# Performance work log

Measured on AMD Instinct MI355X. Metric: run time of the kernel, lower is better.

Reference implementation:

```python
import jax, jax.numpy as jnp
import numpy as np
import math

B, S, D_IN, D_OUT, H = 2, 2048, 1024, 1024, 16
HD = D_OUT // H


def setup_inputs() -> dict:
    key = jax.random.key(0)
    ks = jax.random.split(key, 6)
    scale = 0.02
    return {
        "x": jax.random.normal(ks[0], (B, S, D_IN), dtype=jnp.float32),
        "Wq": jax.random.normal(ks[1], (D_IN, D_OUT), dtype=jnp.float32) * scale,
        "Wk": jax.random.normal(ks[2], (D_IN, D_OUT), dtype=jnp.float32) * scale,
        "Wv": jax.random.normal(ks[3], (D_IN, D_OUT), dtype=jnp.float32) * scale,
        "Wo": jax.random.normal(ks[4], (D_OUT, D_OUT), dtype=jnp.float32) * scale,
        "bo": jax.random.normal(ks[5], (D_OUT,), dtype=jnp.float32) * scale,
    }


def reference(x, Wq, Wk, Wv, Wo, bo):
    b, n, _ = x.shape
    # project and split heads -> [b, h, n, hd]
    q = (x @ Wq).reshape(b, n, H, HD).transpose(0, 2, 1, 3)
    k = (x @ Wk).reshape(b, n, H, HD).transpose(0, 2, 1, 3)
    v = (x @ Wv).reshape(b, n, H, HD).transpose(0, 2, 1, 3)
    # materialized [b, h, n, n] scores with causal mask (as in original)
    scores = jnp.einsum('bhqd,bhkd->bhqk', q, k)
    causal = jnp.tril(jnp.ones((n, n), dtype=bool))  # True = keep
    scores = jnp.where(causal, scores, -jnp.inf)
    attn = jax.nn.softmax(scores / math.sqrt(HD), axis=-1)
    ctx = jnp.einsum('bhqk,bhkd->bhqd', attn, v)
    ctx = ctx.transpose(0, 2, 1, 3).reshape(b, n, D_OUT)
    return ctx @ Wo + bo
```

## Files before the change

kernel.cpp:

```cpp
#include <hip/hip_runtime.h>
#include <hip/hip_bf16.h>
#include <math.h>

typedef __bf16 v8bf __attribute__((ext_vector_type(8)));
typedef __bf16 v4bf __attribute__((ext_vector_type(4)));
typedef short  v4s  __attribute__((ext_vector_type(4)));
typedef float  v4f  __attribute__((ext_vector_type(4)));
typedef unsigned short u16;

static_assert(sizeof(v8bf) == 16, "v8bf must be 16B");

__device__ __forceinline__ u16 f2bf(float f) {
  __hip_bfloat16 h = __float2bfloat16(f);
  return *reinterpret_cast<u16*>(&h);
}
__device__ __forceinline__ v4f mfma16(v8bf a, v8bf b, v4f c) {
  return __builtin_amdgcn_mfma_f32_16x16x32_bf16(a, b, c, 0, 0, 0);
}
__device__ __forceinline__ v4f mfma16k16(v4bf a, v4bf b, v4f c) {
#if __has_builtin(__builtin_amdgcn_mfma_f32_16x16x16_bf16)
  return __builtin_amdgcn_mfma_f32_16x16x16_bf16(a, b, c, 0, 0, 0);
#else
  union { v4bf f; v4s s; } ua, ub;
  ua.f = a; ub.f = b;
  return __builtin_amdgcn_mfma_f32_16x16x16bf16_1k(ua.s, ub.s, c, 0, 0, 0);
#endif
}
__device__ __forceinline__ void async16(const u16* g, u16* l) {
  __builtin_amdgcn_global_load_lds(
      (__attribute__((address_space(1))) void*)(void*)g,
      (__attribute__((address_space(3))) void*)l, 16, 0, 0);
}

__global__ void prep(const float* __restrict__ x, const float* __restrict__ Wq,
                     const float* __restrict__ Wk, const float* __restrict__ Wv,
                     const float* __restrict__ Wo, u16* __restrict__ Wt,
                     u16* __restrict__ xb) {
  int tx = threadIdx.x, ty = threadIdx.y;
  if (blockIdx.z == 4) {
    int bid = blockIdx.y * 32 + blockIdx.x;
    int i = (bid * 1024 + ty * 32 + tx) * 4;
    float4 v = *(const float4*)(x + i);
    ushort4 o;
    o.x = f2bf(v.x); o.y = f2bf(v.y); o.z = f2bf(v.z); o.w = f2bf(v.w);
    *(ushort4*)(xb + i) = o;
    return;
  }
  __shared__ float tile[32][33];
  const float* src = (blockIdx.z == 0) ? Wq : (blockIdx.z == 1) ? Wk : (blockIdx.z == 2) ? Wv : Wo;
  int k0 = blockIdx.x * 32, n0 = blockIdx.y * 32;
  tile[ty][tx] = src[(size_t)(k0 + ty) * 1024 + n0 + tx];
  __syncthreads();
  Wt[(size_t)(blockIdx.z * 1024 + n0 + ty) * 1024 + k0 + tx] = f2bf(tile[tx][ty]);
}

__device__ __forceinline__ void gemm_core(const u16* __restrict__ A, const u16* __restrict__ Bt,
                                          u16* sA, u16* sB, v4f acc[4][4], int bm, int bn) {
  const int t = threadIdx.x;
  const int w = t >> 6, l = t & 63;
  const int quad = l >> 4, low = l & 15;
  const int wm = (w & 1) * 64, wn = (w >> 1) * 64;
  const int rowA = bm * 128 + w * 32 + (l >> 2);
  const int rowB = bn * 128 + w * 32 + (l >> 2);
  const int col8 = (l & 3) * 8;
  u16* la = sA + w * 1024;
  u16* lb = sB + w * 1024;

  for (int kb = 0; kb < 1024; kb += 32) {
    async16(A + (size_t)rowA * 1024 + kb + col8, la);
    async16(A + (size_t)(rowA + 16) * 1024 + kb + col8, la + 512);
    async16(Bt + (size_t)rowB * 1024 + kb + col8, lb);
    async16(Bt + (size_t)(rowB + 16) * 1024 + kb + col8, lb + 512);
    __syncthreads();
    v8bf af[4], bfr[4];
#pragma unroll
    for (int i = 0; i < 4; i++)
      af[i] = *(const v8bf*)(sA + (wm + i * 16 + low) * 32 + quad * 8);
#pragma unroll
    for (int j = 0; j < 4; j++)
      bfr[j] = *(const v8bf*)(sB + (wn + j * 16 + low) * 32 + quad * 8);
#pragma unroll
    for (int i = 0; i < 4; i++)
#pragma unroll
      for (int j = 0; j < 4; j++)
        acc[i][j] = mfma16(af[i], bfr[j], acc[i][j]);
    __syncthreads();
  }
}

__global__ __launch_bounds__(256) void gemm_qkv(const u16* __restrict__ xb,
                                                const u16* __restrict__ Wt,
                                                u16* __restrict__ Qb,
                                                u16* __restrict__ Kb,
                                                u16* __restrict__ Vt) {
  __shared__ __align__(16) u16 sA[128 * 32];
  __shared__ __align__(16) u16 sB[128 * 32];
  v4f acc[4][4] = {};
  const int bm = blockIdx.x, bn = blockIdx.y;
  gemm_core(xb, Wt, sA, sB, acc, bm, bn);
  const int t = threadIdx.x, w = t >> 6, l = t & 63, quad = l >> 4, low = l & 15;
  const int wm = (w & 1) * 64, wn = (w >> 1) * 64;
  const int zone = (bn * 128) >> 10;
  const float qsc = (zone == 0) ? 0.18033688011112042f : 1.0f;
#pragma unroll
  for (int i = 0; i < 4; i++) {
    int m0 = bm * 128 + wm + i * 16 + quad * 4;
#pragma unroll
    for (int j = 0; j < 4; j++) {
      int nn = (bn * 128 + wn + j * 16 + low) & 1023;
      if (zone == 0) {
#pragma unroll
        for (int r = 0; r < 4; r++)
          Qb[(size_t)(m0 + r) * 1024 + nn] = f2bf(acc[i][j][r] * qsc);
      } else if (zone == 1) {
#pragma unroll
        for (int r = 0; r < 4; r++)
          Kb[(size_t)(m0 + r) * 1024 + nn] = f2bf(acc[i][j][r]);
      } else {
        int bb = m0 >> 11, s = m0 & 2047;
#pragma unroll
        for (int r = 0; r < 4; r++)
          Vt[(size_t)(bb * 1024 + nn) * 2048 + s + r] = f2bf(acc[i][j][r]);
      }
    }
  }
}

__global__ __launch_bounds__(256) void gemm_out(const u16* __restrict__ ctx,
                                                const u16* __restrict__ Wt,
                                                const float* __restrict__ bo,
                                                float* __restrict__ out) {
  __shared__ __align__(16) u16 sA[128 * 32];
  __shared__ __align__(16) u16 sB[64 * 32];
  const u16* Bt = Wt + (size_t)3072 * 1024;
  v4f acc[4][2] = {};
  const int bm = blockIdx.x, bn = blockIdx.y;
  const int t = threadIdx.x, w = t >> 6, l = t & 63, quad = l >> 4, low = l & 15;
  const int wm = (w & 1) * 64, wn = (w >> 1) * 32;
  const int rowA = bm * 128 + w * 32 + (l >> 2);
  const int rowB = bn * 64 + w * 16 + (l >> 2);
  const int col8 = (l & 3) * 8;
  u16* la = sA + w * 1024;
  u16* lb = sB + w * 512;

  for (int kb = 0; kb < 1024; kb += 32) {
    async16(ctx + (size_t)rowA * 1024 + kb + col8, la);
    async16(ctx + (size_t)(rowA + 16) * 1024 + kb + col8, la + 512);
    async16(Bt + (size_t)rowB * 1024 + kb + col8, lb);
    __syncthreads();
    v8bf af[4], bfr[2];
#pragma unroll
    for (int i = 0; i < 4; i++)
      af[i] = *(const v8bf*)(sA + (wm + i * 16 + low) * 32 + quad * 8);
#pragma unroll
    for (int j = 0; j < 2; j++)
      bfr[j] = *(const v8bf*)(sB + (wn + j * 16 + low) * 32 + quad * 8);
#pragma unroll
    for (int i = 0; i < 4; i++)
#pragma unroll
      for (int j = 0; j < 2; j++)
        acc[i][j] = mfma16(af[i], bfr[j], acc[i][j]);
    __syncthreads();
  }
#pragma unroll
  for (int i = 0; i < 4; i++) {
    int m0 = bm * 128 + wm + i * 16 + quad * 4;
#pragma unroll
    for (int j = 0; j < 2; j++) {
      int n = bn * 64 + wn + j * 16 + low;
      float bias = bo[n];
#pragma unroll
      for (int r = 0; r < 4; r++)
        out[(size_t)(m0 + r) * 1024 + n] = acc[i][j][r] + bias;
    }
  }
}

__global__ __launch_bounds__(256) void attn(const u16* __restrict__ Qb,
                                            const u16* __restrict__ Kb,
                                            const u16* __restrict__ Vt,
                                            u16* __restrict__ ctx) {
  __shared__ __align__(16) u16 sK[2][4096];
  __shared__ __align__(16) u16 sV[2][4096];
  const int t = threadIdx.x, w = t >> 6, l = t & 63, quad = l >> 4, low = l & 15;
  const int h = blockIdx.x, tile = 31 - blockIdx.y, b = blockIdx.z;
  const int qw = tile * 64 + w * 16;
  const int nkt = tile + 1;

  const u16* kbase = Kb + (size_t)(b * 2048) * 1024 + h * 64;
  const u16* vbase = Vt + (size_t)(b * 1024 + h * 64) * 2048;

  const int srow = l >> 3;
  const int cg = (l & 7) ^ srow;

  const u16* qrow_p = Qb + (size_t)(b * 2048 + qw + low) * 1024 + h * 64;
  v8bf qa0 = *(const v8bf*)(qrow_p + quad * 8);
  v8bf qa1 = *(const v8bf*)(qrow_p + 32 + quad * 8);

  float li = 0.f;
  v4f o[4] = {};

  {
    const u16* kg = kbase + (size_t)(w * 8 + srow) * 1024 + cg * 8;
    async16(kg, &sK[0][w * 512]);
    async16(kg + (size_t)32 * 1024, &sK[0][2048 + w * 512]);
    const u16* vg = vbase + (size_t)(w * 8 + srow) * 2048 + cg * 8;
    async16(vg, &sV[0][w * 512]);
    async16(vg + (size_t)32 * 2048, &sV[0][2048 + w * 512]);
  }

  for (int it = 0; it < nkt; it++) {
    __syncthreads();
    const int kb = it * 64;
    const int cur = it & 1;
    if (it + 1 < nkt) {
      const int nb = (it + 1) & 1;
      const u16* kg = kbase + (size_t)(kb + 64 + w * 8 + srow) * 1024 + cg * 8;
      async16(kg, &sK[nb][w * 512]);
      async16(kg + (size_t)32 * 1024, &sK[nb][2048 + w * 512]);
      const u16* vg = vbase + (size_t)(w * 8 + srow) * 2048 + kb + 64 + cg * 8;
      async16(vg, &sV[nb][w * 512]);
      async16(vg + (size_t)32 * 2048, &sV[nb][2048 + w * 512]);
    }

    v4f s[4] = {};
#pragma unroll
    for (int cf = 0; cf < 4; cf++) {
      const int key = cf * 16 + low;
      v8bf kf0 = *(const v8bf*)(&sK[cur][key * 64 + ((quad ^ (key & 7)) * 8)]);
      v8bf kf1 = *(const v8bf*)(&sK[cur][key * 64 + (((4 + quad) ^ (key & 7)) * 8)]);
      s[cf] = mfma16(kf0, qa0, s[cf]);
      s[cf] = mfma16(kf1, qa1, s[cf]);
    }

    const bool dm = (it == nkt - 1);
    const int qr = qw + low;
    v4bf pf[4];
#pragma unroll
    for (int cf = 0; cf < 4; cf++)
#pragma unroll
      for (int r = 0; r < 4; r++) {
        float e = __builtin_amdgcn_exp2f(s[cf][r]);
        if (dm && (kb + cf * 16 + quad * 4 + r > qr)) e = 0.f;
        li += e;
        pf[cf][r] = (__bf16)e;
      }

#pragma unroll
    for (int df = 0; df < 4; df++) {
      const int d = df * 16 + low;
#pragma unroll
      for (int cf = 0; cf < 4; cf++) {
        const int c = cf * 2 + (quad >> 1);
        const v4bf vf = *(const v4bf*)(&sV[cur][d * 64 + ((c ^ (d & 7)) * 8) + (quad & 1) * 4]);
        o[df] = mfma16k16(pf[cf], vf, o[df]);
      }
    }
  }

  li += __shfl_xor(li, 16);
  li += __shfl_xor(li, 32);

#pragma unroll
  for (int r = 0; r < 4; r++) {
    float lir = __shfl(li, quad * 4 + r);
    float inv = 1.f / lir;
    int row = b * 2048 + qw + quad * 4 + r;
#pragma unroll
    for (int df = 0; df < 4; df++)
      ctx[(size_t)row * 1024 + h * 64 + df * 16 + low] = f2bf(o[df][r] * inv);
  }
}

extern "C" void kernel_launch(void* const* d_in, const int* in_sizes, int n_in,
                              void* d_out, int out_size, void* d_ws, size_t ws_size,
                              hipStream_t stream) {
  const float* x  = (const float*)d_in[0];
  const float* Wq = (const float*)d_in[1];
  const float* Wk = (const float*)d_in[2];
  const float* Wv = (const float*)d_in[3];
  const float* Wo = (const float*)d_in[4];
  const float* bo = (const float*)d_in[5];
  float* out = (float*)d_out;

  char* ws = (char*)d_ws;
  u16* xb  = (u16*)(ws);
  u16* Wt  = (u16*)(ws + 8ull * 1024 * 1024);
  u16* Qb  = (u16*)(ws + 16ull * 1024 * 1024);
  u16* Kb  = (u16*)(ws + 24ull * 1024 * 1024);
  u16* Vt  = (u16*)(ws + 32ull * 1024 * 1024);
  u16* ctx = (u16*)(ws + 40ull * 1024 * 1024);

  prep<<<dim3(32, 32, 5), dim3(32, 32, 1), 0, stream>>>(x, Wq, Wk, Wv, Wo, Wt, xb);
  gemm_qkv<<<dim3(32, 24, 1), dim3(256, 1, 1), 0, stream>>>(xb, Wt, Qb, Kb, Vt);
  attn<<<dim3(16, 32, 2), dim3(256, 1, 1), 0, stream>>>(Qb, Kb, Vt, ctx);
  gemm_out<<<dim3(32, 16, 1), dim3(256, 1, 1), 0, stream>>>(ctx, Wt, bo, out);
}
```

Baseline: 175.6 us.

## Give each attention wave two 16-row query groups, halving block size

The attention kernel now runs 2 waves per block instead of 4, and each wave handles 32 query rows (two 16-row MFMA groups) rather than 16. Each K and V fragment read from shared memory is reused across both groups, which halves LDS read traffic per MFMA. Each wave now issues more async loads per tile. The cost is more registers per wave (doubled accumulators and score tiles) and fewer waves per block to hide latency.

```diff
diff --git a/kernel.cpp b/kernel.cpp
--- a/kernel.cpp
+++ b/kernel.cpp
@@ -176,7 +176,7 @@
   }
 }
 
-__global__ __launch_bounds__(256) void attn(const u16* __restrict__ Qb,
+__global__ __launch_bounds__(128) void attn(const u16* __restrict__ Qb,
                                             const u16* __restrict__ Kb,
                                             const u16* __restrict__ Vt,
                                             u16* __restrict__ ctx) {
@@ -184,7 +184,7 @@
   __shared__ __align__(16) u16 sV[2][4096];
   const int t = threadIdx.x, w = t >> 6, l = t & 63, quad = l >> 4, low = l & 15;
   const int h = blockIdx.x, tile = 31 - blockIdx.y, b = blockIdx.z;
-  const int qw = tile * 64 + w * 16;
+  const int qw = tile * 64 + w * 32;
   const int nkt = tile + 1;
 
   const u16* kbase = Kb + (size_t)(b * 2048) * 1024 + h * 64;
@@ -193,20 +193,24 @@
   const int srow = l >> 3;
   const int cg = (l & 7) ^ srow;
 
-  const u16* qrow_p = Qb + (size_t)(b * 2048 + qw + low) * 1024 + h * 64;
-  v8bf qa0 = *(const v8bf*)(qrow_p + quad * 8);
-  v8bf qa1 = *(const v8bf*)(qrow_p + 32 + quad * 8);
-
-  float li = 0.f;
-  v4f o[4] = {};
+  v8bf qa[2][2];
+#pragma unroll
+  for (int mg = 0; mg < 2; mg++) {
+    const u16* qp = Qb + (size_t)(b * 2048 + qw + mg * 16 + low) * 1024 + h * 64;
+    qa[mg][0] = *(const v8bf*)(qp + quad * 8);
+    qa[mg][1] = *(const v8bf*)(qp + 32 + quad * 8);
+  }
+
+  float li[2] = {0.f, 0.f};
+  v4f o[2][4] = {};
 
   {
-    const u16* kg = kbase + (size_t)(w * 8 + srow) * 1024 + cg * 8;
-    async16(kg, &sK[0][w * 512]);
-    async16(kg + (size_t)32 * 1024, &sK[0][2048 + w * 512]);
-    const u16* vg = vbase + (size_t)(w * 8 + srow) * 2048 + cg * 8;
-    async16(vg, &sV[0][w * 512]);
-    async16(vg + (size_t)32 * 2048, &sV[0][2048 + w * 512]);
+#pragma unroll
+    for (int ss = 0; ss < 4; ss++) {
+      const int row = w * 32 + ss * 8 + srow;
+      async16(kbase + (size_t)row * 1024 + cg * 8, &sK[0][w * 2048 + ss * 512]);
+      async16(vbase + (size_t)row * 2048 + cg * 8, &sV[0][w * 2048 + ss * 512]);
+    }
   }
 
   for (int it = 0; it < nkt; it++) {
@@ -215,36 +219,42 @@
     const int cur = it & 1;
     if (it + 1 < nkt) {
       const int nb = (it + 1) & 1;
-      const u16* kg = kbase + (size_t)(kb + 64 + w * 8 + srow) * 1024 + cg * 8;
-      async16(kg, &sK[nb][w * 512]);
-      async16(kg + (size_t)32 * 1024, &sK[nb][2048 + w * 512]);
-      const u16* vg = vbase + (size_t)(w * 8 + srow) * 2048 + kb + 64 + cg * 8;
-      async16(vg, &sV[nb][w * 512]);
-      async16(vg + (size_t)32 * 2048, &sV[nb][2048 + w * 512]);
-    }
-
-    v4f s[4] = {};
+#pragma unroll
+      for (int ss = 0; ss < 4; ss++) {
+        const int row = w * 32 + ss * 8 + srow;
+        async16(kbase + (size_t)(kb + 64 + row) * 1024 + cg * 8, &sK[nb][w * 2048 + ss * 512]);
+        async16(vbase + (size_t)row * 2048 + kb + 64 + cg * 8, &sV[nb][w * 2048 + ss * 512]);
+      }
+    }
+
+    v4f s[2][4] = {};
 #pragma unroll
     for (int cf = 0; cf < 4; cf++) {
       const int key = cf * 16 + low;
       v8bf kf0 = *(const v8bf*)(&sK[cur][key * 64 + ((quad ^ (key & 7)) * 8)]);
       v8bf kf1 = *(const v8bf*)(&sK[cur][key * 64 + (((4 + quad) ^ (key & 7)) * 8)]);
-      s[cf] = mfma16(kf0, qa0, s[cf]);
-      s[cf] = mfma16(kf1, qa1, s[cf]);
+#pragma unroll
+      for (int mg = 0; mg < 2; mg++) {
+        s[mg][cf] = mfma16(kf0, qa[mg][0], s[mg][cf]);
+        s[mg][cf] = mfma16(kf1, qa[mg][1], s[mg][cf]);
+      }
     }
 
     const bool dm = (it == nkt - 1);
-    const int qr = qw + low;
-    v4bf pf[4];
-#pragma unroll
-    for (int cf = 0; cf < 4; cf++)
-#pragma unroll
-      for (int r = 0; r < 4; r++) {
-        float e = __builtin_amdgcn_exp2f(s[cf][r]);
-        if (dm && (kb + cf * 16 + quad * 4 + r > qr)) e = 0.f;
-        li += e;
-        pf[cf][r] = (__bf16)e;
-      }
+    v4bf pf[2][4];
+#pragma unroll
+    for (int mg = 0; mg < 2; mg++) {
+      const int qr = qw + mg * 16 + low;
+#pragma unroll
+      for (int cf = 0; cf < 4; cf++)
+#pragma unroll
+        for (int r = 0; r < 4; r++) {
+          float e = __builtin_amdgcn_exp2f(s[mg][cf][r]);
+          if (dm && (kb + cf * 16 + quad * 4 + r > qr)) e = 0.f;
+          li[mg] += e;
+          pf[mg][cf][r] = (__bf16)e;
+        }
+    }
 
 #pragma unroll
     for (int df = 0; df < 4; df++) {
@@ -253,23 +263,30 @@
       for (int cf = 0; cf < 4; cf++) {
         const int c = cf * 2 + (quad >> 1);
         const v4bf vf = *(const v4bf*)(&sV[cur][d * 64 + ((c ^ (d & 7)) * 8) + (quad & 1) * 4]);
-        o[df] = mfma16k16(pf[cf], vf, o[df]);
+#pragma unroll
+        for (int mg = 0; mg < 2; mg++)
+          o[mg][df] = mfma16k16(pf[mg][cf], vf, o[mg][df]);
       }
     }
   }
 
-  li += __shfl_xor(li, 16);
-  li += __shfl_xor(li, 32);
-
-#pragma unroll
-  for (int r = 0; r < 4; r++) {
-    float lir = __shfl(li, quad * 4 + r);
-    float inv = 1.f / lir;
-    int row = b * 2048 + qw + quad * 4 + r;
-#pragma unroll
-    for (int df = 0; df < 4; df++)
-      ctx[(size_t)row * 1024 + h * 64 + df * 16 + low] = f2bf(o[df][r] * inv);
-  }
+#pragma unroll
+  for (int mg = 0; mg < 2; mg++) {
+    li[mg] += __shfl_xor(li[mg], 16);
+    li[mg] += __shfl_xor(li[mg], 32);
+  }
+
+#pragma unroll
+  for (int mg = 0; mg < 2; mg++)
+#pragma unroll
+    for (int r = 0; r < 4; r++) {
+      float lir = __shfl(li[mg], quad * 4 + r);
+      float inv = 1.f / lir;
+      int row = b * 2048 + qw + mg * 16 + quad * 4 + r;
+#pragma unroll
+      for (int df = 0; df < 4; df++)
+        ctx[(size_t)row * 1024 + h * 64 + df * 16 + low] = f2bf(o[mg][df][r] * inv);
+    }
 }
 
 extern "C" void kernel_launch(void* const* d_in, const int* in_sizes, int n_in,
@@ -293,6 +310,6 @@
 
   prep<<<dim3(32, 32, 5), dim3(32, 32, 1), 0, stream>>>(x, Wq, Wk, Wv, Wo, Wt, xb);
   gemm_qkv<<<dim3(32, 24, 1), dim3(256, 1, 1), 0, stream>>>(xb, Wt, Qb, Kb, Vt);
-  attn<<<dim3(16, 32, 2), dim3(256, 1, 1), 0, stream>>>(Qb, Kb, Vt, ctx);
+  attn<<<dim3(16, 32, 2), dim3(128, 1, 1), 0, stream>>>(Qb, Kb, Vt, ctx);
   gemm_out<<<dim3(32, 16, 1), dim3(256, 1, 1), 0, stream>>>(ctx, Wt, bo, out);
 }
```

After: 192.6 us. 1.1x slower.
